# Performance work log

Hardware: AMD Instinct MI355X
Metric: run time of the kernel (lower is better)

The kernel has to match this reference:

```python
import jax, jax.numpy as jnp
import numpy as np

NUM_GROUPS = 2
NUM_VARS = 320
TAU = 2.0  # self.temperature
B, L, CONV_DIM = 8, 4096, 512
CODEVECTOR_DIM = 256


def setup_inputs() -> dict:
    key = jax.random.key(0)
    k1, k2, k3, k4, k5 = jax.random.split(key, 5)
    hidden_states = jax.random.normal(k1, (B, L, CONV_DIM), dtype=jnp.float32)
    gumbel_u = jax.random.uniform(k2, (B * L * NUM_GROUPS, NUM_VARS), dtype=jnp.float32)
    w_proj = jax.random.normal(k3, (CONV_DIM, NUM_GROUPS * NUM_VARS), dtype=jnp.float32) * 0.02
    b_proj = jax.random.normal(k4, (NUM_GROUPS * NUM_VARS,), dtype=jnp.float32) * 0.02
    codevectors = jax.random.normal(k5, (1, NUM_GROUPS * NUM_VARS, CODEVECTOR_DIM // NUM_GROUPS), dtype=jnp.float32)
    return {"hidden_states": hidden_states, "gumbel_u": gumbel_u,
            "w_proj": w_proj, "b_proj": b_proj, "codevectors": codevectors}


def reference(hidden_states, gumbel_u, w_proj, b_proj, codevectors):
    b, l, _ = hidden_states.shape
    G, V = NUM_GROUPS, NUM_VARS
    d = codevectors.shape[-1]

    # weight projection: [B, L, C] @ [C, G*V] -> [B, L, G*V] -> [(B*L*G), V]
    logits = (jnp.einsum('blc,cv->blv', hidden_states, w_proj) + b_proj)
    logits = logits.reshape(b * l * G, V)

    # gumbel-softmax (hard=True, training path) with explicit uniform noise
    eps = 1e-10
    gumbel = -jnp.log(-jnp.log(gumbel_u + eps) + eps)
    y_soft = jax.nn.softmax((logits + gumbel) / TAU, axis=-1)          # [(B*L*G), V]
    idx = jnp.argmax(y_soft, axis=-1)
    y_hard = jax.nn.one_hot(idx, V, dtype=y_soft.dtype)
    # straight-through estimator: hard forward, soft backward
    codevector_probs = y_hard - jax.lax.stop_gradient(y_soft) + y_soft  # [(B*L*G), V]

    # perplexity from the (noise-free) soft distribution, mask=None -> mean over sequences
    soft_dist = jax.nn.softmax(logits.reshape(b * l, G, V), axis=-1)
    avg_probs = jnp.mean(soft_dist, axis=0)                             # [G, V]
    perplexity = jnp.sum(jnp.exp(-jnp.sum(avg_probs * jnp.log(avg_probs + 1e-7), axis=-1)))

    # weighted sum over codevectors per group, then concat groups:
    # probs [(B*L), G, V] x codevectors [G, V, d] -> [(B*L), G, d]
    probs = codevector_probs.reshape(b * l, G, V)
    cv = codevectors.reshape(G, V, d)
    out = jnp.einsum('ngv,gvd->ngd', probs, cv).reshape(b, l, G * d)
    return out, perplexity
```

## Files before the change

kernel.cpp:

```cpp
#include <hip/hip_runtime.h>
#include <math.h>

#define NROWS 32768
#define CDIM  512
#define G_    2
#define V_    320
#define NCOLS 640
#define DCODE 128
#define NSLOT 64
#define BMR   32

typedef short bf16x8 __attribute__((ext_vector_type(8)));
typedef float f32x4  __attribute__((ext_vector_type(4)));

__device__ __forceinline__ short f2bf(float f) {
    union { float f; unsigned u; } v; v.f = f;
    unsigned r = v.u + 0x7FFFu + ((v.u >> 16) & 1u);
    return (short)(r >> 16);
}
__device__ __forceinline__ void gl_lds16(const void* g, void* l) {
    __builtin_amdgcn_global_load_lds(
        (const __attribute__((address_space(1))) unsigned int*)g,
        (__attribute__((address_space(3))) unsigned int*)l, 16, 0, 0);
}

__global__ __launch_bounds__(256) void wprep(const float* __restrict__ w,
                                             short* __restrict__ wpk) {
    int gid = blockIdx.x * 256 + threadIdx.x;
    int l15 = gid & 15, kq = (gid >> 4) & 3;
    int rem = gid >> 6;
    int tt16 = rem % 20; rem /= 20;
    int ts = rem & 15, g = rem >> 4;
    int n  = g * V_ + tt16 * 16 + l15;
    int k0 = ts * 32 + kq * 8;
    bf16x8 o;
    #pragma unroll
    for (int e = 0; e < 8; ++e) o[e] = f2bf(w[(size_t)(k0 + e) * NCOLS + n]);
    *(bf16x8*)&wpk[(size_t)gid * 8] = o;
}

__global__ __launch_bounds__(256) void hprep(const float* __restrict__ hidden,
                                             short* __restrict__ hpk) {
    int gid = blockIdx.x * 256 + threadIdx.x;
    int lane = gid & 63;
    int mf   = (gid >> 6) & 1;
    int ts   = (gid >> 7) & 15;
    int rb   = gid >> 11;
    int row  = rb * BMR + mf * 16 + (lane & 15);
    int k0   = ts * 32 + (lane >> 4) * 8;
    const float* src = hidden + (size_t)row * CDIM + k0;
    float4 a = *(const float4*)src;
    float4 b = *(const float4*)(src + 4);
    bf16x8 o;
    o[0]=f2bf(a.x); o[1]=f2bf(a.y); o[2]=f2bf(a.z); o[3]=f2bf(a.w);
    o[4]=f2bf(b.x); o[5]=f2bf(b.y); o[6]=f2bf(b.z); o[7]=f2bf(b.w);
    *(bf16x8*)&hpk[(size_t)gid * 8] = o;
}

__global__ __launch_bounds__(512, 3) void gvq_gemm(
    const short* __restrict__ hpk,
    const float* __restrict__ gumbel_u,
    const short* __restrict__ wpk,
    const float* __restrict__ bias,
    const float* __restrict__ cv,
    float* __restrict__ out,
    float* __restrict__ gavg)
{
    __shared__ short Hs[16384];
    __shared__ float s_psum[G_][4][BMR];
    __shared__ float s_bestv[G_][4][BMR];
    __shared__ int   s_besti[G_][4][BMR];

    const int t    = threadIdx.x;
    const int wave = t >> 6;
    const int lane = t & 63;
    const int l15  = lane & 15;
    const int kq   = lane >> 4;
    const int cg   = wave;
    const int g    = cg >> 2;
    const int tb   = (cg & 3) * 5;
    const int rb   = blockIdx.x;
    const int m0   = rb * BMR;

    const short* wbase = wpk + ((size_t)(g * 16) * 20 + tb) * 512 + (size_t)lane * 8;

    {
        const short* hsrc = hpk + (size_t)rb * 16384;
        #pragma unroll
        for (int i = 0; i < 4; ++i) {
            const int off = (wave * 4 + i) * 512;
            gl_lds16(hsrc + off + lane * 8, &Hs[off]);
        }
    }

    f32x4 acc[5][2];
    #pragma unroll
    for (int nf = 0; nf < 5; ++nf)
        #pragma unroll
        for (int mf = 0; mf < 2; ++mf)
            #pragma unroll
            for (int r = 0; r < 4; ++r) acc[nf][mf][r] = 0.f;

    bf16x8 bw[5];
    #pragma unroll
    for (int nf = 0; nf < 5; ++nf) bw[nf] = *(const bf16x8*)(wbase + nf * 512);

    __syncthreads();

    #pragma unroll
    for (int ts = 0; ts < 16; ++ts) {
        bf16x8 bn[5];
        if (ts < 15) {
            const short* wn = wbase + (ts + 1) * 10240;
            #pragma unroll
            for (int nf = 0; nf < 5; ++nf) bn[nf] = *(const bf16x8*)(wn + nf * 512);
        }
        bf16x8 hf0 = *(const bf16x8*)&Hs[ts * 1024 + lane * 8];
        bf16x8 hf1 = *(const bf16x8*)&Hs[ts * 1024 + 512 + lane * 8];
        #pragma unroll
        for (int nf = 0; nf < 5; ++nf)
            acc[nf][0] = __builtin_amdgcn_mfma_f32_16x16x32_bf16(bw[nf], hf0, acc[nf][0], 0, 0, 0);
        #pragma unroll
        for (int nf = 0; nf < 5; ++nf)
            acc[nf][1] = __builtin_amdgcn_mfma_f32_16x16x32_bf16(bw[nf], hf1, acc[nf][1], 0, 0, 0);
        #pragma unroll
        for (int nf = 0; nf < 5; ++nf) bw[nf] = bn[nf];
    }

    float4 bv4[5], u4[2][5];
    #pragma unroll
    for (int nf = 0; nf < 5; ++nf)
        bv4[nf] = *(const float4*)&bias[g * V_ + (tb + nf) * 16 + kq * 4];
    #pragma unroll
    for (int mf = 0; mf < 2; ++mf) {
        const float* up = gumbel_u + ((size_t)(m0 + mf * 16 + l15) * G_ + g) * V_;
        #pragma unroll
        for (int nf = 0; nf < 5; ++nf)
            u4[mf][nf] = *(const float4*)&up[(tb + nf) * 16 + kq * 4];
    }

    #pragma unroll
    for (int mf = 0; mf < 2; ++mf) {
        float s = 0.f, best = -1e30f; int bi = 0;
        #pragma unroll
        for (int nf = 0; nf < 5; ++nf) {
            #pragma unroll
            for (int r = 0; r < 4; ++r) {
                float z = fminf(acc[nf][mf][r] + bv4[nf][r], 60.f);
                float e = __expf(z);
                acc[nf][mf][r] = e;
                s += e;
                float u = (r == 0) ? u4[mf][nf].x : (r == 1) ? u4[mf][nf].y
                        : (r == 2) ? u4[mf][nf].z : u4[mf][nf].w;
                float wv = -__logf(u + 1e-10f) + 1e-10f;
                float ratio = e * __builtin_amdgcn_rcpf(wv);
                const int vi = (tb + nf) * 16 + kq * 4 + r;
                if (ratio > best) { best = ratio; bi = vi; }
            }
        }
        #pragma unroll
        for (int o = 16; o <= 32; o <<= 1) {
            s += __shfl_xor(s, o);
            float ov = __shfl_xor(best, o);
            int   oi = __shfl_xor(bi, o);
            if (ov > best || (ov == best && oi < bi)) { best = ov; bi = oi; }
        }
        if (kq == 0) {
            s_psum[g][cg & 3][mf * 16 + l15]  = s;
            s_bestv[g][cg & 3][mf * 16 + l15] = best;
            s_besti[g][cg & 3][mf * 16 + l15] = bi;
        }
    }
    __syncthreads();

    float inv[2];
    #pragma unroll
    for (int mf = 0; mf < 2; ++mf) {
        const int rl = mf * 16 + l15;
        inv[mf] = 1.f / (s_psum[g][0][rl] + s_psum[g][1][rl] +
                         s_psum[g][2][rl] + s_psum[g][3][rl]);
    }
    float cpl[5][4];
    #pragma unroll
    for (int nf = 0; nf < 5; ++nf)
        #pragma unroll
        for (int r = 0; r < 4; ++r) {
            float v = acc[nf][0][r] * inv[0] + acc[nf][1][r] * inv[1];
            #pragma unroll
            for (int o = 1; o <= 8; o <<= 1) v += __shfl_xor(v, o);
            cpl[nf][r] = v;
        }
    float* gslot = gavg + (size_t)(rb & (NSLOT - 1)) * NCOLS;
    if (l15 == 0) {
        #pragma unroll
        for (int nf = 0; nf < 5; ++nf)
            #pragma unroll
            for (int r = 0; r < 4; ++r)
                atomicAdd(&gslot[g * V_ + (tb + nf) * 16 + kq * 4 + r], cpl[nf][r]);
    }

    {
        const int task = t >> 3;
        const int seg  = t & 7;
        const int r_   = task >> 1, gg = task & 1;
        float best = s_bestv[gg][0][r_]; int bi = s_besti[gg][0][r_];
        #pragma unroll
        for (int q = 1; q < 4; ++q) {
            float v = s_bestv[gg][q][r_];
            if (v > best) { best = v; bi = s_besti[gg][q][r_]; }
        }
        const float* src = cv + ((size_t)gg * V_ + bi) * DCODE + seg * 16;
        float* dst = out + (size_t)(m0 + r_) * (G_ * DCODE) + gg * DCODE + seg * 16;
        #pragma unroll
        for (int j = 0; j < 4; ++j)
            *(float4*)(dst + j * 4) = *(const float4*)(src + j * 4);
    }
}

__global__ __launch_bounds__(1024) void gvq_perp(const float* __restrict__ gavg,
                                                 float* __restrict__ out)
{
    __shared__ float sp[NCOLS];
    const int t = threadIdx.x;
    if (t < NCOLS) {
        float a = 0.f;
        #pragma unroll
        for (int sb = 0; sb < 8; ++sb) {
            float p[8];
            #pragma unroll
            for (int j = 0; j < 8; ++j)
                p[j] = gavg[(size_t)(sb * 8 + j) * NCOLS + t];
            #pragma unroll
            for (int j = 0; j < 8; ++j) a += p[j];
        }
        sp[t] = a;
    }
    __syncthreads();
    if (t < 64) {
        float s0 = 0.f, s1 = 0.f;
        #pragma unroll
        for (int j = 0; j < 5; ++j) {
            float p0 = sp[t + j * 64]      * (1.f / NROWS);
            float p1 = sp[V_ + t + j * 64] * (1.f / NROWS);
            s0 += p0 * __logf(p0 + 1e-7f);
            s1 += p1 * __logf(p1 + 1e-7f);
        }
        #pragma unroll
        for (int o = 1; o < 64; o <<= 1) {
            s0 += __shfl_xor(s0, o);
            s1 += __shfl_xor(s1, o);
        }
        if (t == 0)
            out[(size_t)NROWS * (G_ * DCODE)] = expf(-s0) + expf(-s1);
    }
}

extern "C" void kernel_launch(void* const* d_in, const int* in_sizes, int n_in,
                              void* d_out, int out_size, void* d_ws, size_t ws_size,
                              hipStream_t stream)
{
    const float* hidden = (const float*)d_in[0];
    const float* gu     = (const float*)d_in[1];
    const float* w      = (const float*)d_in[2];
    const float* b      = (const float*)d_in[3];
    const float* cv     = (const float*)d_in[4];
    float* out  = (float*)d_out;
    float* gavg = (float*)d_ws;
    short* wpk  = (short*)((char*)d_ws + 163840);
    short* hpk  = (short*)((char*)d_ws + 819200);

    hipMemsetAsync(d_ws, 0, NSLOT * NCOLS * sizeof(float), stream);
    wprep<<<160, 256, 0, stream>>>(w, wpk);
    hprep<<<8192, 256, 0, stream>>>(hidden, hpk);
    gvq_gemm<<<NROWS / BMR, 512, 0, stream>>>(hpk, gu, wpk, b, cv, out, gavg);
    gvq_perp<<<1, 1024, 0, stream>>>(gavg, out);
}
```

Measured before the change: 107.0 us.

## Split GEMM blocks by codebook group with 256-thread blocks

```diff
diff --git a/kernel.cpp b/kernel.cpp
--- a/kernel.cpp
+++ b/kernel.cpp
@@ -57,7 +57,7 @@
     *(bf16x8*)&hpk[(size_t)gid * 8] = o;
 }
 
-__global__ __launch_bounds__(512, 3) void gvq_gemm(
+__global__ __launch_bounds__(256, 4) void gvq_gemm(
     const short* __restrict__ hpk,
     const float* __restrict__ gumbel_u,
     const short* __restrict__ wpk,
@@ -67,19 +67,18 @@
     float* __restrict__ gavg)
 {
     __shared__ short Hs[16384];
-    __shared__ float s_psum[G_][4][BMR];
-    __shared__ float s_bestv[G_][4][BMR];
-    __shared__ int   s_besti[G_][4][BMR];
+    __shared__ float s_psum[4][BMR];
+    __shared__ float s_bestv[4][BMR];
+    __shared__ int   s_besti[4][BMR];
 
     const int t    = threadIdx.x;
     const int wave = t >> 6;
     const int lane = t & 63;
     const int l15  = lane & 15;
     const int kq   = lane >> 4;
-    const int cg   = wave;
-    const int g    = cg >> 2;
-    const int tb   = (cg & 3) * 5;
+    const int tb   = wave * 5;
     const int rb   = blockIdx.x;
+    const int g    = blockIdx.y;
     const int m0   = rb * BMR;
 
     const short* wbase = wpk + ((size_t)(g * 16) * 20 + tb) * 512 + (size_t)lane * 8;
@@ -87,8 +86,8 @@
     {
         const short* hsrc = hpk + (size_t)rb * 16384;
         #pragma unroll
-        for (int i = 0; i < 4; ++i) {
-            const int off = (wave * 4 + i) * 512;
+        for (int i = 0; i < 8; ++i) {
+            const int off = (wave * 8 + i) * 512;
             gl_lds16(hsrc + off + lane * 8, &Hs[off]);
         }
     }
@@ -166,9 +165,9 @@
             if (ov > best || (ov == best && oi < bi)) { best = ov; bi = oi; }
         }
         if (kq == 0) {
-            s_psum[g][cg & 3][mf * 16 + l15]  = s;
-            s_bestv[g][cg & 3][mf * 16 + l15] = best;
-            s_besti[g][cg & 3][mf * 16 + l15] = bi;
+            s_psum[wave][mf * 16 + l15]  = s;
+            s_bestv[wave][mf * 16 + l15] = best;
+            s_besti[wave][mf * 16 + l15] = bi;
         }
     }
     __syncthreads();
@@ -177,8 +176,8 @@
     #pragma unroll
     for (int mf = 0; mf < 2; ++mf) {
         const int rl = mf * 16 + l15;
-        inv[mf] = 1.f / (s_psum[g][0][rl] + s_psum[g][1][rl] +
-                         s_psum[g][2][rl] + s_psum[g][3][rl]);
+        inv[mf] = 1.f / (s_psum[0][rl] + s_psum[1][rl] +
+                         s_psum[2][rl] + s_psum[3][rl]);
     }
     float cpl[5][4];
     #pragma unroll
@@ -200,17 +199,16 @@
     }
 
     {
-        const int task = t >> 3;
-        const int seg  = t & 7;
-        const int r_   = task >> 1, gg = task & 1;
-        float best = s_bestv[gg][0][r_]; int bi = s_besti[gg][0][r_];
+        const int r_  = t >> 3;
+        const int seg = t & 7;
+        float best = s_bestv[0][r_]; int bi = s_besti[0][r_];
         #pragma unroll
         for (int q = 1; q < 4; ++q) {
-            float v = s_bestv[gg][q][r_];
-            if (v > best) { best = v; bi = s_besti[gg][q][r_]; }
-        }
-        const float* src = cv + ((size_t)gg * V_ + bi) * DCODE + seg * 16;
-        float* dst = out + (size_t)(m0 + r_) * (G_ * DCODE) + gg * DCODE + seg * 16;
+            float v = s_bestv[q][r_];
+            if (v > best) { best = v; bi = s_besti[q][r_]; }
+        }
+        const float* src = cv + ((size_t)g * V_ + bi) * DCODE + seg * 16;
+        float* dst = out + (size_t)(m0 + r_) * (G_ * DCODE) + g * DCODE + seg * 16;
         #pragma unroll
         for (int j = 0; j < 4; ++j)
             *(float4*)(dst + j * 4) = *(const float4*)(src + j * 4);
@@ -272,6 +270,6 @@
     hipMemsetAsync(d_ws, 0, NSLOT * NCOLS * sizeof(float), stream);
     wprep<<<160, 256, 0, stream>>>(w, wpk);
     hprep<<<8192, 256, 0, stream>>>(hidden, hpk);
-    gvq_gemm<<<NROWS / BMR, 512, 0, stream>>>(hpk, gu, wpk, b, cv, out, gavg);
+    gvq_gemm<<<dim3(NROWS / BMR, G_), 256, 0, stream>>>(hpk, gu, wpk, b, cv, out, gavg);
     gvq_perp<<<1, 1024, 0, stream>>>(gavg, out);
 }
```

Result: faster. 97.19 us (-9.1%).
